# Performance work log

Measured on AMD Instinct MI355X. Metric: run time of the kernel, lower is better.

The kernel has to match this reference:

```python
import jax, jax.numpy as jnp
import numpy as np

D_MODEL = 256
D_INNER = 512   # expand_factor * d_model
D_STATE = 64
DT_RANK = 4     # ceil(d_model / 64)
D_CONV = 4
B = 8
L = 144


def setup_inputs() -> dict:
    key = jax.random.key(0)
    ks = jax.random.split(key, 8)
    s = lambda k, shp, sc=0.02: jax.random.normal(k, shp, jnp.float32) * sc
    x = jax.random.normal(ks[0], (B, L, D_MODEL), jnp.float32)
    lastin = jnp.zeros((B, D_INNER, D_STATE), jnp.float32)  # accepted but unused by the scan
    W_in = s(ks[1], (2 * D_INNER, D_MODEL))              # in_proj (no bias)
    conv_w = s(ks[2], (D_INNER, 1, D_CONV), 0.1)          # depthwise conv kernel [O, I/groups, K]
    conv_b = jnp.zeros((D_INNER,), jnp.float32)
    W_x = s(ks[3], (DT_RANK + 2 * D_STATE, D_INNER))      # x_proj (no bias)
    W_dt = s(ks[4], (D_INNER, DT_RANK), 0.1)
    b_dt = jnp.full((D_INNER,), -4.0, jnp.float32)        # softplus -> small dt, like mamba init
    A_log = jnp.log(jnp.tile(jnp.arange(1, D_STATE + 1, dtype=jnp.float32), (D_INNER, 1)))
    Dp = jnp.ones((D_INNER,), jnp.float32)
    W_out = s(ks[5], (D_MODEL, D_INNER))                  # out_proj (no bias)
    return dict(x=x, lastin=lastin, W_in=W_in, conv_w=conv_w, conv_b=conv_b,
                W_x=W_x, W_dt=W_dt, b_dt=b_dt, A_log=A_log, Dp=Dp, W_out=W_out)


def _forward(x, lastin, W_in, conv_w, conv_b, W_x, W_dt, b_dt, A_log, Dp, W_out):
    # in_proj and split
    xz = jnp.einsum('bld,ed->ble', x, W_in)               # [B, L, 2*d_inner]
    ix, z = jnp.split(xz, 2, axis=-1)

    # depthwise causal-ish conv1d: torch padding=2 then slice [:L] == padding (2, 1)
    ix = jnp.swapaxes(ix, 1, 2)                            # [B, d_inner, L]
    ix = jax.lax.conv_general_dilated(
        ix, conv_w, window_strides=(1,), padding=[(2, 1)],
        feature_group_count=D_INNER, dimension_numbers=('NCH', 'OIH', 'NCH'))
    ix = ix + conv_b[None, :, None]
    ix = jnp.swapaxes(ix, 1, 2)                            # [B, L, d_inner]
    ix = jax.nn.silu(ix)

    # ssm parameterization
    A = -jnp.exp(A_log)                                    # [d_inner, d_state]
    dBC = jnp.einsum('bld,ed->ble', ix, W_x)               # [B, L, dt_rank + 2*d_state]
    dt_r = dBC[..., :DT_RANK]
    Bm = dBC[..., DT_RANK:DT_RANK + D_STATE]               # [B, L, d_state]
    Cm = dBC[..., DT_RANK + D_STATE:]                      # [B, L, d_state]
    delta = jax.nn.softplus(jnp.einsum('blr,dr->bld', dt_r, W_dt) + b_dt)  # [B, L, d_inner]

    # discretization
    deltaA = jnp.exp(delta[..., None] * A)                 # [B, L, d_inner, d_state]
    BX = (delta * ix)[..., None] * Bm[:, :, None, :]       # [B, L, d_inner, d_state]

    # sequential selective scan: h_t = deltaA_t * h_{t-1} + BX_t
    def step(h, inp):
        dA_t, bx_t = inp
        h = dA_t * h + bx_t
        return h, h

    h0 = jnp.zeros((x.shape[0], D_INNER, D_STATE), x.dtype)
    _, hs = jax.lax.scan(step, h0, (jnp.moveaxis(deltaA, 1, 0), jnp.moveaxis(BX, 1, 0)))
    # hs: [L, B, d_inner, d_state]

    y = jnp.einsum('lbdn,lbn->bld', hs, jnp.moveaxis(Cm, 1, 0))  # [B, L, d_inner]
    y = y + Dp * ix

    out = jnp.einsum('bld,ed->ble', y * jax.nn.silu(z), W_out)   # [B, L, d_model]
    return out


def reference(x, lastin, W_in, conv_w, conv_b, W_x, W_dt, b_dt, A_log, Dp, W_out):
    return _forward(x, lastin, W_in, conv_w, conv_b, W_x, W_dt, b_dt, A_log, Dp, W_out)
```

## Files before the change

### kernel.cpp

```cpp
#include <hip/hip_runtime.h>
#include <hip/hip_bf16.h>

#define B_SZ 8
#define L_SEQ 144
#define NTOK 1152
#define D_MODEL 256
#define D_INNER 512
#define D_STATE 64
#define DT_RANK 4

#define BM 64
#define BN 64
#define BK 16

template<bool A_MK, bool B_NK, bool GN>
__global__ __launch_bounds__(256) void gemm_k(const float* __restrict__ A,
                                              const float* __restrict__ Bm,
                                              float* __restrict__ C,
                                              const int M, const int N, const int K,
                                              const int lda, const int ldb, const int ldc,
                                              const int kslab, const size_t sstride) {
    __shared__ float As[BK][BM + 4];
    __shared__ float Bs[BK][BN + 4];
    const int tid = threadIdx.x;
    const int m0 = blockIdx.y * BM;
    const int n0 = blockIdx.x * BN;
    const int kbeg = blockIdx.z * kslab;
    const int kend = kbeg + kslab;
    const int ty = tid >> 4, tx = tid & 15;
    const int lrow = tid >> 2, kq = (tid & 3) * 4;
    const int kk = tid >> 4, cc = (tid & 15) * 4;
    float acc[4][4] = {};

    for (int k0 = kbeg; k0 < kend; k0 += BK) {
        float4 av, bv;
        if (A_MK) av = *(const float4*)(A + (size_t)(m0 + lrow) * lda + k0 + kq);
        else      av = *(const float4*)(A + (size_t)(k0 + kk) * lda + m0 + cc);
        if (B_NK) {
            bv = *(const float4*)(Bm + (size_t)(k0 + kk) * ldb + n0 + cc);
        } else {
            bv = make_float4(0.f, 0.f, 0.f, 0.f);
            if (!GN || (n0 + lrow) < N)
                bv = *(const float4*)(Bm + (size_t)(n0 + lrow) * ldb + k0 + kq);
        }
        __syncthreads();
        if (A_MK) {
            As[kq + 0][lrow] = av.x; As[kq + 1][lrow] = av.y;
            As[kq + 2][lrow] = av.z; As[kq + 3][lrow] = av.w;
        } else {
            *(float4*)&As[kk][cc] = av;
        }
        if (B_NK) {
            *(float4*)&Bs[kk][cc] = bv;
        } else {
            Bs[kq + 0][lrow] = bv.x; Bs[kq + 1][lrow] = bv.y;
            Bs[kq + 2][lrow] = bv.z; Bs[kq + 3][lrow] = bv.w;
        }
        __syncthreads();
#pragma unroll
        for (int k = 0; k < BK; ++k) {
            const float4 a4 = *(const float4*)&As[k][ty * 4];
            const float4 b4 = *(const float4*)&Bs[k][tx * 4];
            const float a_[4] = {a4.x, a4.y, a4.z, a4.w};
            const float b_[4] = {b4.x, b4.y, b4.z, b4.w};
#pragma unroll
            for (int i = 0; i < 4; ++i)
#pragma unroll
                for (int j = 0; j < 4; ++j)
                    acc[i][j] = fmaf(a_[i], b_[j], acc[i][j]);
        }
    }
    C += (size_t)blockIdx.z * sstride;
#pragma unroll
    for (int i = 0; i < 4; ++i) {
        const int gm = m0 + ty * 4 + i;
        const int gn = n0 + tx * 4;
        if (!GN || gn < N)
            *(float4*)(C + (size_t)gm * ldc + gn) =
                make_float4(acc[i][0], acc[i][1], acc[i][2], acc[i][3]);
    }
}

__global__ __launch_bounds__(256) void reduce4_k(const float4* __restrict__ in,
                                                 float4* __restrict__ out,
                                                 const int n4, const int s4) {
    const int i = blockIdx.x * 256 + threadIdx.x;
    if (i >= n4) return;
    const float4 a = in[i], b = in[i + s4], c = in[i + 2 * s4], d = in[i + 3 * s4];
    out[i] = make_float4(a.x + b.x + c.x + d.x, a.y + b.y + c.y + d.y,
                         a.z + b.z + c.z + d.z, a.w + b.w + c.w + d.w);
}

__global__ __launch_bounds__(128) void conv_k(const float* __restrict__ xzT,
                                              const float* __restrict__ cw,
                                              const float* __restrict__ cb,
                                              float* __restrict__ ixT) {
    const int tok = blockIdx.x * 128 + threadIdx.x;
    const int d = blockIdx.y;
    const int b = tok / L_SEQ;
    const int t = tok - b * L_SEQ;
    const float* row = xzT + (size_t)d * NTOK + tok;
    const float4 w = *(const float4*)(cw + d * 4);
    float s = cb[d];
    if (t >= 2) s = fmaf(w.x, row[-2], s);
    if (t >= 1) s = fmaf(w.y, row[-1], s);
    s = fmaf(w.z, row[0], s);
    if (t < L_SEQ - 1) s = fmaf(w.w, row[1], s);
    ixT[(size_t)d * NTOK + tok] = s * __builtin_amdgcn_rcpf(1.f + __expf(-s));
}

template<int CNT>
__device__ __forceinline__ void scan_chunk(const float* __restrict__ dBC,
                                           const float* __restrict__ xzT,
                                           const float* __restrict__ ixT,
                                           float* __restrict__ gT,
                                           float4* __restrict__ aux_w,
                                           float (*__restrict__ Pw)[65],
                                           const int d, const int base, const int t0,
                                           const float An2, const float4 wdt,
                                           const float bdt, const float dpv,
                                           const int lane, float& h) {
    if (lane < CNT) {
        const int tok = base + t0 + lane;
        const float4 dt4 = *(const float4*)(dBC + (size_t)tok * 132);
        float s = fmaf(dt4.x, wdt.x, bdt);
        s = fmaf(dt4.y, wdt.y, s);
        s = fmaf(dt4.z, wdt.z, s);
        s = fmaf(dt4.w, wdt.w, s);
        const float delta = fmaxf(s, 0.f) + __logf(1.f + __expf(-fabsf(s)));
        const float ixv = ixT[(size_t)d * NTOK + tok];
        const float zv  = xzT[(size_t)(D_INNER + d) * NTOK + tok];
        const float sz  = zv * __builtin_amdgcn_rcpf(1.f + __expf(-zv));
        aux_w[lane] = make_float4(delta, delta * ixv, dpv * ixv, sz);
    }
#pragma unroll 8
    for (int i = 0; i < CNT; ++i) {
        const size_t rb = (size_t)(base + t0 + i) * 132;
        const float Bv = dBC[rb + DT_RANK + lane];
        const float Cv = dBC[rb + DT_RANK + D_STATE + lane];
        const float4 a4 = aux_w[i];
        const float dA = __builtin_amdgcn_exp2f(a4.x * An2);
        h = fmaf(dA, h, a4.y * Bv);
        Pw[i][lane] = h * Cv;
    }
    const int tl = lane & 31, hf = lane >> 5;
    float s2 = 0.f;
    if (tl < CNT) {
#pragma unroll
        for (int j = 0; j < 32; ++j) s2 += Pw[tl][hf * 32 + j];
    }
    s2 += __shfl_xor(s2, 32, 64);
    if (hf == 0 && tl < CNT) {
        const float4 a4 = aux_w[tl];
        gT[(size_t)d * NTOK + base + t0 + tl] = (s2 + a4.z) * a4.w;
    }
}

__global__ __launch_bounds__(256) void scan_k(const float* __restrict__ dBC,
                                              const float* __restrict__ xzT,
                                              const float* __restrict__ ixT,
                                              const float* __restrict__ W_dt,
                                              const float* __restrict__ b_dt,
                                              const float* __restrict__ A_log,
                                              const float* __restrict__ Dp,
                                              float* __restrict__ gT) {
    __shared__ float4 aux_s[4][32];
    __shared__ float P[4][32][65];
    const int w = threadIdx.x >> 6, lane = threadIdx.x & 63;
    const int b = blockIdx.x >> 7, dg = blockIdx.x & 127;
    const int d = (dg << 2) | w;
    const int base = b * L_SEQ;
    const float An2 = -__expf(A_log[(d << 6) + lane]) * 1.44269504088896f;
    const float4 wdt = *(const float4*)(W_dt + (d << 2));
    const float bdt = b_dt[d], dpv = Dp[d];
    float h = 0.f;
    scan_chunk<32>(dBC, xzT, ixT, gT, aux_s[w], P[w], d, base, 0,  An2, wdt, bdt, dpv, lane, h);
    scan_chunk<32>(dBC, xzT, ixT, gT, aux_s[w], P[w], d, base, 32, An2, wdt, bdt, dpv, lane, h);
    scan_chunk<32>(dBC, xzT, ixT, gT, aux_s[w], P[w], d, base, 64, An2, wdt, bdt, dpv, lane, h);
    scan_chunk<32>(dBC, xzT, ixT, gT, aux_s[w], P[w], d, base, 96, An2, wdt, bdt, dpv, lane, h);
    scan_chunk<16>(dBC, xzT, ixT, gT, aux_s[w], P[w], d, base, 128, An2, wdt, bdt, dpv, lane, h);
}

extern "C" void kernel_launch(void* const* d_in, const int* in_sizes, int n_in,
                              void* d_out, int out_size, void* d_ws, size_t ws_size,
                              hipStream_t stream) {
    const float* x      = (const float*)d_in[0];
    const float* W_in   = (const float*)d_in[2];
    const float* conv_w = (const float*)d_in[3];
    const float* conv_b = (const float*)d_in[4];
    const float* W_x    = (const float*)d_in[5];
    const float* W_dt   = (const float*)d_in[6];
    const float* b_dt   = (const float*)d_in[7];
    const float* A_log  = (const float*)d_in[8];
    const float* Dp     = (const float*)d_in[9];
    const float* W_out  = (const float*)d_in[10];
    float* out = (float*)d_out;

    float* ws    = (float*)d_ws;
    float* xzT   = ws;
    float* ixT   = xzT + 1179648;
    float* dBC   = ixT + 589824;
    float* gT    = dBC + 152064;
    float* slab3 = gT + 589824;
    float* slab6 = xzT;

    gemm_k<true, false, false><<<dim3(18, 16, 1), 256, 0, stream>>>(
        W_in, x, xzT, 1024, NTOK, D_MODEL, D_MODEL, D_MODEL, NTOK, D_MODEL, 0);
    conv_k<<<dim3(9, D_INNER), 128, 0, stream>>>(xzT, conv_w, conv_b, ixT);
    gemm_k<false, false, true><<<dim3(3, 18, 4), 256, 0, stream>>>(
        ixT, W_x, slab3, NTOK, 132, D_INNER, NTOK, D_INNER, 132, 128, (size_t)NTOK * 132);
    reduce4_k<<<dim3(149), 256, 0, stream>>>((const float4*)slab3, (float4*)dBC,
                                             NTOK * 132 / 4, NTOK * 132 / 4);
    scan_k<<<dim3(B_SZ * 128), 256, 0, stream>>>(dBC, xzT, ixT, W_dt, b_dt, A_log, Dp, gT);
    gemm_k<false, false, false><<<dim3(4, 18, 4), 256, 0, stream>>>(
        gT, W_out, slab6, NTOK, D_MODEL, D_INNER, NTOK, D_INNER, D_MODEL, 128,
        (size_t)NTOK * D_MODEL);
    reduce4_k<<<dim3(288), 256, 0, stream>>>((const float4*)slab6, (float4*)out,
                                             NTOK * D_MODEL / 4, NTOK * D_MODEL / 4);
}
```

Baseline: 142.5 us.

## Fuse all stages into one cooperative persistent kernel with grid syncs

Replaces the seven separate launches with a single cooperative kernel that walks the in_proj GEMM, conv, x_proj GEMM, reduction, scan, out_proj GEMM and final reduction as grid-strided job loops separated by grid.sync. The goal is to remove per-launch overhead and inter-kernel gaps. The change also adds register prefetch of the next K-tile in the GEMM tile and uses 8-way split-K instead of 4-way for the two smaller GEMMs. Grid barriers and persistent-grid occupancy limits may cost more than the launch gaps they remove. A fallback multi-kernel path stays in place for when the cooperative launch fails.

```diff
diff --git a/kernel.cpp b/kernel.cpp
--- a/kernel.cpp
+++ b/kernel.cpp
@@ -1,5 +1,7 @@
 #include <hip/hip_runtime.h>
-#include <hip/hip_bf16.h>
+#include <hip/hip_cooperative_groups.h>
+
+namespace cg = cooperative_groups;
 
 #define B_SZ 8
 #define L_SEQ 144
@@ -8,41 +10,34 @@
 #define D_INNER 512
 #define D_STATE 64
 #define DT_RANK 4
+#define NDBC 132
 
 #define BM 64
 #define BN 64
 #define BK 16
 
-template<bool A_MK, bool B_NK, bool GN>
-__global__ __launch_bounds__(256) void gemm_k(const float* __restrict__ A,
-                                              const float* __restrict__ Bm,
-                                              float* __restrict__ C,
-                                              const int M, const int N, const int K,
-                                              const int lda, const int ldb, const int ldc,
-                                              const int kslab, const size_t sstride) {
-    __shared__ float As[BK][BM + 4];
-    __shared__ float Bs[BK][BN + 4];
-    const int tid = threadIdx.x;
-    const int m0 = blockIdx.y * BM;
-    const int n0 = blockIdx.x * BN;
-    const int kbeg = blockIdx.z * kslab;
-    const int kend = kbeg + kslab;
+template<bool A_MK, bool GN>
+__device__ __forceinline__ void gemm_tile(const float* __restrict__ A,
+                                          const float* __restrict__ Bm,
+                                          float* __restrict__ C,
+                                          const int N, const int lda, const int ldb,
+                                          const int ldc, const int m0, const int n0,
+                                          const int kbeg, const int kend,
+                                          float (*__restrict__ As)[BM + 4],
+                                          float (*__restrict__ Bs)[BN + 4],
+                                          const int tid) {
     const int ty = tid >> 4, tx = tid & 15;
     const int lrow = tid >> 2, kq = (tid & 3) * 4;
     const int kk = tid >> 4, cc = (tid & 15) * 4;
     float acc[4][4] = {};
+    float4 av, bv;
+    if (A_MK) av = *(const float4*)(A + (size_t)(m0 + lrow) * lda + kbeg + kq);
+    else      av = *(const float4*)(A + (size_t)(kbeg + kk) * lda + m0 + cc);
+    bv = make_float4(0.f, 0.f, 0.f, 0.f);
+    if (!GN || (n0 + lrow) < N)
+        bv = *(const float4*)(Bm + (size_t)(n0 + lrow) * ldb + kbeg + kq);
 
     for (int k0 = kbeg; k0 < kend; k0 += BK) {
-        float4 av, bv;
-        if (A_MK) av = *(const float4*)(A + (size_t)(m0 + lrow) * lda + k0 + kq);
-        else      av = *(const float4*)(A + (size_t)(k0 + kk) * lda + m0 + cc);
-        if (B_NK) {
-            bv = *(const float4*)(Bm + (size_t)(k0 + kk) * ldb + n0 + cc);
-        } else {
-            bv = make_float4(0.f, 0.f, 0.f, 0.f);
-            if (!GN || (n0 + lrow) < N)
-                bv = *(const float4*)(Bm + (size_t)(n0 + lrow) * ldb + k0 + kq);
-        }
         __syncthreads();
         if (A_MK) {
             As[kq + 0][lrow] = av.x; As[kq + 1][lrow] = av.y;
@@ -50,13 +45,16 @@
         } else {
             *(float4*)&As[kk][cc] = av;
         }
-        if (B_NK) {
-            *(float4*)&Bs[kk][cc] = bv;
-        } else {
-            Bs[kq + 0][lrow] = bv.x; Bs[kq + 1][lrow] = bv.y;
-            Bs[kq + 2][lrow] = bv.z; Bs[kq + 3][lrow] = bv.w;
-        }
+        Bs[kq + 0][lrow] = bv.x; Bs[kq + 1][lrow] = bv.y;
+        Bs[kq + 2][lrow] = bv.z; Bs[kq + 3][lrow] = bv.w;
         __syncthreads();
+        const int k1 = k0 + BK;
+        if (k1 < kend) {
+            if (A_MK) av = *(const float4*)(A + (size_t)(m0 + lrow) * lda + k1 + kq);
+            else      av = *(const float4*)(A + (size_t)(k1 + kk) * lda + m0 + cc);
+            if (!GN || (n0 + lrow) < N)
+                bv = *(const float4*)(Bm + (size_t)(n0 + lrow) * ldb + k1 + kq);
+        }
 #pragma unroll
         for (int k = 0; k < BK; ++k) {
             const float4 a4 = *(const float4*)&As[k][ty * 4];
@@ -70,7 +68,6 @@
                     acc[i][j] = fmaf(a_[i], b_[j], acc[i][j]);
         }
     }
-    C += (size_t)blockIdx.z * sstride;
 #pragma unroll
     for (int i = 0; i < 4; ++i) {
         const int gm = m0 + ty * 4 + i;
@@ -79,6 +76,180 @@
             *(float4*)(C + (size_t)gm * ldc + gn) =
                 make_float4(acc[i][0], acc[i][1], acc[i][2], acc[i][3]);
     }
+}
+
+template<int CNT>
+__device__ __forceinline__ void scan_chunk(const float* __restrict__ dBC,
+                                           const float* __restrict__ xzT,
+                                           const float* __restrict__ ixT,
+                                           float* __restrict__ gT,
+                                           float4* __restrict__ aux_w,
+                                           float (*__restrict__ Pw)[65],
+                                           const int d, const int base, const int t0,
+                                           const float An2, const float4 wdt,
+                                           const float bdt, const float dpv,
+                                           const int lane, float& h) {
+    if (lane < CNT) {
+        const int tok = base + t0 + lane;
+        const float4 dt4 = *(const float4*)(dBC + (size_t)tok * NDBC);
+        float s = fmaf(dt4.x, wdt.x, bdt);
+        s = fmaf(dt4.y, wdt.y, s);
+        s = fmaf(dt4.z, wdt.z, s);
+        s = fmaf(dt4.w, wdt.w, s);
+        const float delta = fmaxf(s, 0.f) + __logf(1.f + __expf(-fabsf(s)));
+        const float ixv = ixT[(size_t)d * NTOK + tok];
+        const float zv  = xzT[(size_t)(D_INNER + d) * NTOK + tok];
+        const float sz  = zv * __builtin_amdgcn_rcpf(1.f + __expf(-zv));
+        aux_w[lane] = make_float4(delta, delta * ixv, dpv * ixv, sz);
+    }
+#pragma unroll 8
+    for (int i = 0; i < CNT; ++i) {
+        const size_t rb = (size_t)(base + t0 + i) * NDBC;
+        const float Bv = dBC[rb + DT_RANK + lane];
+        const float Cv = dBC[rb + DT_RANK + D_STATE + lane];
+        const float4 a4 = aux_w[i];
+        const float dA = __builtin_amdgcn_exp2f(a4.x * An2);
+        h = fmaf(dA, h, a4.y * Bv);
+        Pw[i][lane] = h * Cv;
+    }
+    const int tl = lane & 31, hf = lane >> 5;
+    float s2 = 0.f;
+    if (tl < CNT) {
+#pragma unroll
+        for (int j = 0; j < 32; ++j) s2 += Pw[tl][hf * 32 + j];
+    }
+    s2 += __shfl_xor(s2, 32, 64);
+    if (hf == 0 && tl < CNT) {
+        const float4 a4 = aux_w[tl];
+        gT[(size_t)d * NTOK + base + t0 + tl] = (s2 + a4.z) * a4.w;
+    }
+}
+
+union MegaSmem {
+    struct { float As[BK][BM + 4]; float Bs[BK][BN + 4]; } g;
+    struct { float4 aux[4][32]; float P[4][32][65]; } s;
+};
+
+__global__ __launch_bounds__(256, 4) void mega_k(
+    const float* __restrict__ x,      const float* __restrict__ W_in,
+    const float* __restrict__ conv_w, const float* __restrict__ conv_b,
+    const float* __restrict__ W_x,    const float* __restrict__ W_dt,
+    const float* __restrict__ b_dt,   const float* __restrict__ A_log,
+    const float* __restrict__ Dp,     const float* __restrict__ W_out,
+    float* __restrict__ out,          float* __restrict__ ws) {
+    __shared__ MegaSmem sm;
+    cg::grid_group grid = cg::this_grid();
+    const int tid = threadIdx.x;
+    const int bid = blockIdx.x;
+    const int nb  = gridDim.x;
+
+    float* xzT = ws;
+    float* ixT = xzT + 1179648;
+    float* dBC = ixT + 589824;
+    float* gT  = dBC + 152064;
+    float* sl3 = gT + 589824;
+    float* sl6 = sl3 + 8 * 152064;
+
+    for (int job = bid; job < 288; job += nb)
+        gemm_tile<true, false>(W_in, x, xzT, NTOK, D_MODEL, D_MODEL, NTOK,
+                               (job / 18) * BM, (job % 18) * BN, 0, D_MODEL,
+                               sm.g.As, sm.g.Bs, tid);
+    grid.sync();
+
+    for (int idx = bid * 256 + tid; idx < D_INNER * NTOK; idx += nb * 256) {
+        const int dd = idx / NTOK, tok = idx - dd * NTOK;
+        const int bb = tok / L_SEQ, t = tok - bb * L_SEQ;
+        const float* row = xzT + (size_t)dd * NTOK + tok;
+        const float4 wv = *(const float4*)(conv_w + dd * 4);
+        float s = conv_b[dd];
+        if (t >= 2) s = fmaf(wv.x, row[-2], s);
+        if (t >= 1) s = fmaf(wv.y, row[-1], s);
+        s = fmaf(wv.z, row[0], s);
+        if (t < L_SEQ - 1) s = fmaf(wv.w, row[1], s);
+        ixT[idx] = s * __builtin_amdgcn_rcpf(1.f + __expf(-s));
+    }
+    grid.sync();
+
+    for (int job = bid; job < 432; job += nb) {
+        const int sK = job / 54, r = job % 54;
+        gemm_tile<false, true>(ixT, W_x, sl3 + (size_t)sK * 152064, NDBC,
+                               NTOK, D_INNER, NDBC,
+                               (r / 3) * BM, (r % 3) * BN, sK * 64, sK * 64 + 64,
+                               sm.g.As, sm.g.Bs, tid);
+    }
+    grid.sync();
+
+    {
+        const float4* in4 = (const float4*)sl3;
+        float4* o4 = (float4*)dBC;
+        for (int i = bid * 256 + tid; i < 38016; i += nb * 256) {
+            float4 a = in4[i];
+#pragma unroll
+            for (int sK = 1; sK < 8; ++sK) {
+                const float4 bb = in4[i + sK * 38016];
+                a.x += bb.x; a.y += bb.y; a.z += bb.z; a.w += bb.w;
+            }
+            o4[i] = a;
+        }
+    }
+    grid.sync();
+
+    {
+        const int w = tid >> 6, lane = tid & 63;
+        for (int unit = bid; unit < B_SZ * 128; unit += nb) {
+            const int bb = unit >> 7, dg = unit & 127;
+            const int d = (dg << 2) | w;
+            const int base = bb * L_SEQ;
+            const float An2 = -__expf(A_log[(d << 6) + lane]) * 1.44269504088896f;
+            const float4 wdt = *(const float4*)(W_dt + (d << 2));
+            const float bdt = b_dt[d], dpv = Dp[d];
+            float h = 0.f;
+            scan_chunk<32>(dBC, xzT, ixT, gT, sm.s.aux[w], sm.s.P[w], d, base, 0,   An2, wdt, bdt, dpv, lane, h);
+            scan_chunk<32>(dBC, xzT, ixT, gT, sm.s.aux[w], sm.s.P[w], d, base, 32,  An2, wdt, bdt, dpv, lane, h);
+            scan_chunk<32>(dBC, xzT, ixT, gT, sm.s.aux[w], sm.s.P[w], d, base, 64,  An2, wdt, bdt, dpv, lane, h);
+            scan_chunk<32>(dBC, xzT, ixT, gT, sm.s.aux[w], sm.s.P[w], d, base, 96,  An2, wdt, bdt, dpv, lane, h);
+            scan_chunk<16>(dBC, xzT, ixT, gT, sm.s.aux[w], sm.s.P[w], d, base, 128, An2, wdt, bdt, dpv, lane, h);
+        }
+    }
+    grid.sync();
+
+    for (int job = bid; job < 576; job += nb) {
+        const int sK = job / 72, r = job % 72;
+        gemm_tile<false, false>(gT, W_out, sl6 + (size_t)sK * 294912, D_MODEL,
+                                NTOK, D_INNER, D_MODEL,
+                                (r / 4) * BM, (r % 4) * BN, sK * 64, sK * 64 + 64,
+                                sm.g.As, sm.g.Bs, tid);
+    }
+    grid.sync();
+
+    {
+        const float4* in4 = (const float4*)sl6;
+        float4* o4 = (float4*)out;
+        for (int i = bid * 256 + tid; i < 73728; i += nb * 256) {
+            float4 a = in4[i];
+#pragma unroll
+            for (int sK = 1; sK < 8; ++sK) {
+                const float4 bb = in4[i + sK * 73728];
+                a.x += bb.x; a.y += bb.y; a.z += bb.z; a.w += bb.w;
+            }
+            o4[i] = a;
+        }
+    }
+}
+
+template<bool A_MK, bool GN>
+__global__ __launch_bounds__(256) void gemm_k2(const float* __restrict__ A,
+                                               const float* __restrict__ Bm,
+                                               float* __restrict__ C,
+                                               const int N, const int lda, const int ldb,
+                                               const int ldc, const int kslab,
+                                               const size_t sstride) {
+    __shared__ float As[BK][BM + 4];
+    __shared__ float Bs[BK][BN + 4];
+    gemm_tile<A_MK, GN>(A, Bm, C + (size_t)blockIdx.z * sstride, N, lda, ldb, ldc,
+                        blockIdx.y * BM, blockIdx.x * BN,
+                        blockIdx.z * kslab, blockIdx.z * kslab + kslab,
+                        As, Bs, (int)threadIdx.x);
 }
 
 __global__ __launch_bounds__(256) void reduce4_k(const float4* __restrict__ in,
@@ -107,53 +278,6 @@
     s = fmaf(w.z, row[0], s);
     if (t < L_SEQ - 1) s = fmaf(w.w, row[1], s);
     ixT[(size_t)d * NTOK + tok] = s * __builtin_amdgcn_rcpf(1.f + __expf(-s));
-}
-
-template<int CNT>
-__device__ __forceinline__ void scan_chunk(const float* __restrict__ dBC,
-                                           const float* __restrict__ xzT,
-                                           const float* __restrict__ ixT,
-                                           float* __restrict__ gT,
-                                           float4* __restrict__ aux_w,
-                                           float (*__restrict__ Pw)[65],
-                                           const int d, const int base, const int t0,
-                                           const float An2, const float4 wdt,
-                                           const float bdt, const float dpv,
-                                           const int lane, float& h) {
-    if (lane < CNT) {
-        const int tok = base + t0 + lane;
-        const float4 dt4 = *(const float4*)(dBC + (size_t)tok * 132);
-        float s = fmaf(dt4.x, wdt.x, bdt);
-        s = fmaf(dt4.y, wdt.y, s);
-        s = fmaf(dt4.z, wdt.z, s);
-        s = fmaf(dt4.w, wdt.w, s);
-        const float delta = fmaxf(s, 0.f) + __logf(1.f + __expf(-fabsf(s)));
-        const float ixv = ixT[(size_t)d * NTOK + tok];
-        const float zv  = xzT[(size_t)(D_INNER + d) * NTOK + tok];
-        const float sz  = zv * __builtin_amdgcn_rcpf(1.f + __expf(-zv));
-        aux_w[lane] = make_float4(delta, delta * ixv, dpv * ixv, sz);
-    }
-#pragma unroll 8
-    for (int i = 0; i < CNT; ++i) {
-        const size_t rb = (size_t)(base + t0 + i) * 132;
-        const float Bv = dBC[rb + DT_RANK + lane];
-        const float Cv = dBC[rb + DT_RANK + D_STATE + lane];
-        const float4 a4 = aux_w[i];
-        const float dA = __builtin_amdgcn_exp2f(a4.x * An2);
-        h = fmaf(dA, h, a4.y * Bv);
-        Pw[i][lane] = h * Cv;
-    }
-    const int tl = lane & 31, hf = lane >> 5;
-    float s2 = 0.f;
-    if (tl < CNT) {
-#pragma unroll
-        for (int j = 0; j < 32; ++j) s2 += Pw[tl][hf * 32 + j];
-    }
-    s2 += __shfl_xor(s2, 32, 64);
-    if (hf == 0 && tl < CNT) {
-        const float4 a4 = aux_w[tl];
-        gT[(size_t)d * NTOK + base + t0 + tl] = (s2 + a4.z) * a4.w;
-    }
 }
 
 __global__ __launch_bounds__(256) void scan_k(const float* __restrict__ dBC,
@@ -174,10 +298,10 @@
     const float4 wdt = *(const float4*)(W_dt + (d << 2));
     const float bdt = b_dt[d], dpv = Dp[d];
     float h = 0.f;
-    scan_chunk<32>(dBC, xzT, ixT, gT, aux_s[w], P[w], d, base, 0,  An2, wdt, bdt, dpv, lane, h);
-    scan_chunk<32>(dBC, xzT, ixT, gT, aux_s[w], P[w], d, base, 32, An2, wdt, bdt, dpv, lane, h);
-    scan_chunk<32>(dBC, xzT, ixT, gT, aux_s[w], P[w], d, base, 64, An2, wdt, bdt, dpv, lane, h);
-    scan_chunk<32>(dBC, xzT, ixT, gT, aux_s[w], P[w], d, base, 96, An2, wdt, bdt, dpv, lane, h);
+    scan_chunk<32>(dBC, xzT, ixT, gT, aux_s[w], P[w], d, base, 0,   An2, wdt, bdt, dpv, lane, h);
+    scan_chunk<32>(dBC, xzT, ixT, gT, aux_s[w], P[w], d, base, 32,  An2, wdt, bdt, dpv, lane, h);
+    scan_chunk<32>(dBC, xzT, ixT, gT, aux_s[w], P[w], d, base, 64,  An2, wdt, bdt, dpv, lane, h);
+    scan_chunk<32>(dBC, xzT, ixT, gT, aux_s[w], P[w], d, base, 96,  An2, wdt, bdt, dpv, lane, h);
     scan_chunk<16>(dBC, xzT, ixT, gT, aux_s[w], P[w], d, base, 128, An2, wdt, bdt, dpv, lane, h);
 }
 
@@ -195,26 +319,49 @@
     const float* Dp     = (const float*)d_in[9];
     const float* W_out  = (const float*)d_in[10];
     float* out = (float*)d_out;
-
-    float* ws    = (float*)d_ws;
-    float* xzT   = ws;
-    float* ixT   = xzT + 1179648;
-    float* dBC   = ixT + 589824;
-    float* gT    = dBC + 152064;
-    float* slab3 = gT + 589824;
-    float* slab6 = xzT;
-
-    gemm_k<true, false, false><<<dim3(18, 16, 1), 256, 0, stream>>>(
-        W_in, x, xzT, 1024, NTOK, D_MODEL, D_MODEL, D_MODEL, NTOK, D_MODEL, 0);
+    float* ws  = (float*)d_ws;
+
+    static int grid = -1;
+    if (grid < 0) {
+        int occ = 0;
+        if (hipOccupancyMaxActiveBlocksPerMultiprocessor(&occ, (const void*)mega_k,
+                                                         256, 0) != hipSuccess || occ < 1)
+            occ = 1;
+        int dev = 0;
+        hipGetDevice(&dev);
+        int nCU = 0;
+        if (hipDeviceGetAttribute(&nCU, hipDeviceAttributeMultiprocessorCount, dev)
+                != hipSuccess || nCU < 1)
+            nCU = 256;
+        long g = (long)occ * (long)nCU;
+        grid = (int)(g > 1024 ? 1024 : g);
+        if (grid < 1) grid = 256;
+    }
+
+    void* args[] = { (void*)&x, (void*)&W_in, (void*)&conv_w, (void*)&conv_b,
+                     (void*)&W_x, (void*)&W_dt, (void*)&b_dt, (void*)&A_log,
+                     (void*)&Dp, (void*)&W_out, (void*)&out, (void*)&ws };
+    if (hipLaunchCooperativeKernel((const void*)mega_k, dim3(grid), dim3(256),
+                                   args, 0, stream) == hipSuccess)
+        return;
+
+    float* xzT = ws;
+    float* ixT = xzT + 1179648;
+    float* dBC = ixT + 589824;
+    float* gT  = dBC + 152064;
+    float* sl3 = gT + 589824;
+    float* sl6 = sl3 + 8 * 152064;
+
+    gemm_k2<true, false><<<dim3(18, 16, 1), 256, 0, stream>>>(
+        W_in, x, xzT, NTOK, D_MODEL, D_MODEL, NTOK, D_MODEL, 0);
     conv_k<<<dim3(9, D_INNER), 128, 0, stream>>>(xzT, conv_w, conv_b, ixT);
-    gemm_k<false, false, true><<<dim3(3, 18, 4), 256, 0, stream>>>(
-        ixT, W_x, slab3, NTOK, 132, D_INNER, NTOK, D_INNER, 132, 128, (size_t)NTOK * 132);
-    reduce4_k<<<dim3(149), 256, 0, stream>>>((const float4*)slab3, (float4*)dBC,
-                                             NTOK * 132 / 4, NTOK * 132 / 4);
+    gemm_k2<false, true><<<dim3(3, 18, 4), 256, 0, stream>>>(
+        ixT, W_x, sl3, NDBC, NTOK, D_INNER, NDBC, 128, (size_t)NTOK * NDBC);
+    reduce4_k<<<dim3(149), 256, 0, stream>>>((const float4*)sl3, (float4*)dBC,
+                                             38016, 38016);
     scan_k<<<dim3(B_SZ * 128), 256, 0, stream>>>(dBC, xzT, ixT, W_dt, b_dt, A_log, Dp, gT);
-    gemm_k<false, false, false><<<dim3(4, 18, 4), 256, 0, stream>>>(
-        gT, W_out, slab6, NTOK, D_MODEL, D_INNER, NTOK, D_INNER, D_MODEL, 128,
-        (size_t)NTOK * D_MODEL);
-    reduce4_k<<<dim3(288), 256, 0, stream>>>((const float4*)slab6, (float4*)out,
-                                             NTOK * D_MODEL / 4, NTOK * D_MODEL / 4);
-}
+    gemm_k2<false, false><<<dim3(4, 18, 4), 256, 0, stream>>>(
+        gT, W_out, sl6, D_MODEL, NTOK, D_INNER, D_MODEL, 128, (size_t)NTOK * D_MODEL);
+    reduce4_k<<<dim3(288), 256, 0, stream>>>((const float4*)sl6, (float4*)out,
+                                             73728, 73728);
+}
```

Measured after the change: 501.0 us. 3.51x slower.

## Fuse depthwise conv+SiLU into x_proj GEMM load and scan; prefetch GEMM tiles

Applied to the files above, without the earlier changes.

Removes the standalone conv kernel and the ixT intermediate buffer. The x_proj GEMM now applies the depthwise conv and SiLU while loading its A tile, using neighbour reads within each batch sequence. The scan kernel recomputes the same conv+SiLU per token from xzT. The GEMM also prefetches the next K-tile into registers before computing on the current one, overlapping global loads with FMAs. This saves one launch and a full write/read of the activation, at the cost of redundant exp work across N-blocks and in the scan, plus higher register pressure.

```diff
diff --git a/kernel.cpp b/kernel.cpp
--- a/kernel.cpp
+++ b/kernel.cpp
@@ -1,5 +1,4 @@
 #include <hip/hip_runtime.h>
-#include <hip/hip_bf16.h>
 
 #define B_SZ 8
 #define L_SEQ 144
@@ -8,17 +7,20 @@
 #define D_INNER 512
 #define D_STATE 64
 #define DT_RANK 4
+#define NDBC 132
 
 #define BM 64
 #define BN 64
 #define BK 16
 
-template<bool A_MK, bool B_NK, bool GN>
+template<bool A_MK, bool GN, bool CONV>
 __global__ __launch_bounds__(256) void gemm_k(const float* __restrict__ A,
                                               const float* __restrict__ Bm,
                                               float* __restrict__ C,
-                                              const int M, const int N, const int K,
-                                              const int lda, const int ldb, const int ldc,
+                                              const int N, const int lda, const int ldb,
+                                              const int ldc,
+                                              const float* __restrict__ cw,
+                                              const float* __restrict__ cb,
                                               const int kslab, const size_t sstride) {
     __shared__ float As[BK][BM + 4];
     __shared__ float Bs[BK][BN + 4];
@@ -31,32 +33,60 @@
     const int lrow = tid >> 2, kq = (tid & 3) * 4;
     const int kk = tid >> 4, cc = (tid & 15) * 4;
     float acc[4][4] = {};
-
-    for (int k0 = kbeg; k0 < kend; k0 += BK) {
-        float4 av, bv;
-        if (A_MK) av = *(const float4*)(A + (size_t)(m0 + lrow) * lda + k0 + kq);
-        else      av = *(const float4*)(A + (size_t)(k0 + kk) * lda + m0 + cc);
-        if (B_NK) {
-            bv = *(const float4*)(Bm + (size_t)(k0 + kk) * ldb + n0 + cc);
+    float4 av, bv, cw4;
+    float xm2 = 0.f, xm1 = 0.f, xp4 = 0.f, cbv = 0.f;
+
+    auto loadA = [&](const int k0) {
+        if (A_MK) {
+            av = *(const float4*)(A + (size_t)(m0 + lrow) * lda + k0 + kq);
         } else {
-            bv = make_float4(0.f, 0.f, 0.f, 0.f);
-            if (!GN || (n0 + lrow) < N)
-                bv = *(const float4*)(Bm + (size_t)(n0 + lrow) * ldb + k0 + kq);
+            const float* row = A + (size_t)(k0 + kk) * lda + m0 + cc;
+            av = *(const float4*)row;
+            if (CONV) {
+                const int t = (m0 + cc) % L_SEQ;
+                xm2 = (t > 0) ? row[-2] : 0.f;
+                xm1 = (t > 0) ? row[-1] : 0.f;
+                xp4 = (t < L_SEQ - 4) ? row[4] : 0.f;
+                cw4 = *(const float4*)(cw + (k0 + kk) * 4);
+                cbv = cb[k0 + kk];
+            }
         }
-        __syncthreads();
+        if (!GN || (n0 + lrow) < N)
+            bv = *(const float4*)(Bm + (size_t)(n0 + lrow) * ldb + k0 + kq);
+    };
+
+    auto storeLDS = [&]() {
         if (A_MK) {
             As[kq + 0][lrow] = av.x; As[kq + 1][lrow] = av.y;
             As[kq + 2][lrow] = av.z; As[kq + 3][lrow] = av.w;
+        } else if (CONV) {
+            const float in7[7] = {xm2, xm1, av.x, av.y, av.z, av.w, xp4};
+            float4 o;
+            float* op = &o.x;
+#pragma unroll
+            for (int j = 0; j < 4; ++j) {
+                float s = cbv;
+                s = fmaf(cw4.x, in7[j + 0], s);
+                s = fmaf(cw4.y, in7[j + 1], s);
+                s = fmaf(cw4.z, in7[j + 2], s);
+                s = fmaf(cw4.w, in7[j + 3], s);
+                op[j] = s * __builtin_amdgcn_rcpf(1.f + __expf(-s));
+            }
+            *(float4*)&As[kk][cc] = o;
         } else {
             *(float4*)&As[kk][cc] = av;
         }
-        if (B_NK) {
-            *(float4*)&Bs[kk][cc] = bv;
-        } else {
-            Bs[kq + 0][lrow] = bv.x; Bs[kq + 1][lrow] = bv.y;
-            Bs[kq + 2][lrow] = bv.z; Bs[kq + 3][lrow] = bv.w;
-        }
+        Bs[kq + 0][lrow] = bv.x; Bs[kq + 1][lrow] = bv.y;
+        Bs[kq + 2][lrow] = bv.z; Bs[kq + 3][lrow] = bv.w;
+    };
+
+    bv = make_float4(0.f, 0.f, 0.f, 0.f);
+    loadA(kbeg);
+    for (int k0 = kbeg; k0 < kend; k0 += BK) {
         __syncthreads();
+        storeLDS();
+        __syncthreads();
+        if (k0 + BK < kend) loadA(k0 + BK);
 #pragma unroll
         for (int k = 0; k < BK; ++k) {
             const float4 a4 = *(const float4*)&As[k][ty * 4];
@@ -91,51 +121,41 @@
                          a.z + b.z + c.z + d.z, a.w + b.w + c.w + d.w);
 }
 
-__global__ __launch_bounds__(128) void conv_k(const float* __restrict__ xzT,
-                                              const float* __restrict__ cw,
-                                              const float* __restrict__ cb,
-                                              float* __restrict__ ixT) {
-    const int tok = blockIdx.x * 128 + threadIdx.x;
-    const int d = blockIdx.y;
-    const int b = tok / L_SEQ;
-    const int t = tok - b * L_SEQ;
-    const float* row = xzT + (size_t)d * NTOK + tok;
-    const float4 w = *(const float4*)(cw + d * 4);
-    float s = cb[d];
-    if (t >= 2) s = fmaf(w.x, row[-2], s);
-    if (t >= 1) s = fmaf(w.y, row[-1], s);
-    s = fmaf(w.z, row[0], s);
-    if (t < L_SEQ - 1) s = fmaf(w.w, row[1], s);
-    ixT[(size_t)d * NTOK + tok] = s * __builtin_amdgcn_rcpf(1.f + __expf(-s));
-}
-
 template<int CNT>
 __device__ __forceinline__ void scan_chunk(const float* __restrict__ dBC,
                                            const float* __restrict__ xzT,
-                                           const float* __restrict__ ixT,
                                            float* __restrict__ gT,
                                            float4* __restrict__ aux_w,
                                            float (*__restrict__ Pw)[65],
                                            const int d, const int base, const int t0,
                                            const float An2, const float4 wdt,
                                            const float bdt, const float dpv,
+                                           const float4 cw4, const float cbv,
                                            const int lane, float& h) {
     if (lane < CNT) {
-        const int tok = base + t0 + lane;
-        const float4 dt4 = *(const float4*)(dBC + (size_t)tok * 132);
+        const int t = t0 + lane;
+        const int tok = base + t;
+        const float* row = xzT + (size_t)d * NTOK + tok;
+        float s0 = cbv;
+        if (t >= 2) s0 = fmaf(cw4.x, row[-2], s0);
+        if (t >= 1) s0 = fmaf(cw4.y, row[-1], s0);
+        s0 = fmaf(cw4.z, row[0], s0);
+        if (t < L_SEQ - 1) s0 = fmaf(cw4.w, row[1], s0);
+        const float ixv = s0 * __builtin_amdgcn_rcpf(1.f + __expf(-s0));
+
+        const float4 dt4 = *(const float4*)(dBC + (size_t)tok * NDBC);
         float s = fmaf(dt4.x, wdt.x, bdt);
         s = fmaf(dt4.y, wdt.y, s);
         s = fmaf(dt4.z, wdt.z, s);
         s = fmaf(dt4.w, wdt.w, s);
         const float delta = fmaxf(s, 0.f) + __logf(1.f + __expf(-fabsf(s)));
-        const float ixv = ixT[(size_t)d * NTOK + tok];
-        const float zv  = xzT[(size_t)(D_INNER + d) * NTOK + tok];
-        const float sz  = zv * __builtin_amdgcn_rcpf(1.f + __expf(-zv));
+        const float zv = xzT[(size_t)(D_INNER + d) * NTOK + tok];
+        const float sz = zv * __builtin_amdgcn_rcpf(1.f + __expf(-zv));
         aux_w[lane] = make_float4(delta, delta * ixv, dpv * ixv, sz);
     }
 #pragma unroll 8
     for (int i = 0; i < CNT; ++i) {
-        const size_t rb = (size_t)(base + t0 + i) * 132;
+        const size_t rb = (size_t)(base + t0 + i) * NDBC;
         const float Bv = dBC[rb + DT_RANK + lane];
         const float Cv = dBC[rb + DT_RANK + D_STATE + lane];
         const float4 a4 = aux_w[i];
@@ -158,11 +178,12 @@
 
 __global__ __launch_bounds__(256) void scan_k(const float* __restrict__ dBC,
                                               const float* __restrict__ xzT,
-                                              const float* __restrict__ ixT,
                                               const float* __restrict__ W_dt,
                                               const float* __restrict__ b_dt,
                                               const float* __restrict__ A_log,
                                               const float* __restrict__ Dp,
+                                              const float* __restrict__ conv_w,
+                                              const float* __restrict__ conv_b,
                                               float* __restrict__ gT) {
     __shared__ float4 aux_s[4][32];
     __shared__ float P[4][32][65];
@@ -173,12 +194,14 @@
     const float An2 = -__expf(A_log[(d << 6) + lane]) * 1.44269504088896f;
     const float4 wdt = *(const float4*)(W_dt + (d << 2));
     const float bdt = b_dt[d], dpv = Dp[d];
+    const float4 cw4 = *(const float4*)(conv_w + (d << 2));
+    const float cbv = conv_b[d];
     float h = 0.f;
-    scan_chunk<32>(dBC, xzT, ixT, gT, aux_s[w], P[w], d, base, 0,  An2, wdt, bdt, dpv, lane, h);
-    scan_chunk<32>(dBC, xzT, ixT, gT, aux_s[w], P[w], d, base, 32, An2, wdt, bdt, dpv, lane, h);
-    scan_chunk<32>(dBC, xzT, ixT, gT, aux_s[w], P[w], d, base, 64, An2, wdt, bdt, dpv, lane, h);
-    scan_chunk<32>(dBC, xzT, ixT, gT, aux_s[w], P[w], d, base, 96, An2, wdt, bdt, dpv, lane, h);
-    scan_chunk<16>(dBC, xzT, ixT, gT, aux_s[w], P[w], d, base, 128, An2, wdt, bdt, dpv, lane, h);
+    scan_chunk<32>(dBC, xzT, gT, aux_s[w], P[w], d, base, 0,   An2, wdt, bdt, dpv, cw4, cbv, lane, h);
+    scan_chunk<32>(dBC, xzT, gT, aux_s[w], P[w], d, base, 32,  An2, wdt, bdt, dpv, cw4, cbv, lane, h);
+    scan_chunk<32>(dBC, xzT, gT, aux_s[w], P[w], d, base, 64,  An2, wdt, bdt, dpv, cw4, cbv, lane, h);
+    scan_chunk<32>(dBC, xzT, gT, aux_s[w], P[w], d, base, 96,  An2, wdt, bdt, dpv, cw4, cbv, lane, h);
+    scan_chunk<16>(dBC, xzT, gT, aux_s[w], P[w], d, base, 128, An2, wdt, bdt, dpv, cw4, cbv, lane, h);
 }
 
 extern "C" void kernel_launch(void* const* d_in, const int* in_sizes, int n_in,
@@ -196,25 +219,25 @@
     const float* W_out  = (const float*)d_in[10];
     float* out = (float*)d_out;
 
-    float* ws    = (float*)d_ws;
-    float* xzT   = ws;
-    float* ixT   = xzT + 1179648;
-    float* dBC   = ixT + 589824;
-    float* gT    = dBC + 152064;
-    float* slab3 = gT + 589824;
-    float* slab6 = xzT;
+    float* ws  = (float*)d_ws;
+    float* xzT = ws;
+    float* dBC = xzT + 1179648;
+    float* gT  = dBC + 152064;
+    float* sl3 = gT + 589824;
+    float* sl6 = xzT;
 
     gemm_k<true, false, false><<<dim3(18, 16, 1), 256, 0, stream>>>(
-        W_in, x, xzT, 1024, NTOK, D_MODEL, D_MODEL, D_MODEL, NTOK, D_MODEL, 0);
-    conv_k<<<dim3(9, D_INNER), 128, 0, stream>>>(xzT, conv_w, conv_b, ixT);
-    gemm_k<false, false, true><<<dim3(3, 18, 4), 256, 0, stream>>>(
-        ixT, W_x, slab3, NTOK, 132, D_INNER, NTOK, D_INNER, 132, 128, (size_t)NTOK * 132);
-    reduce4_k<<<dim3(149), 256, 0, stream>>>((const float4*)slab3, (float4*)dBC,
-                                             NTOK * 132 / 4, NTOK * 132 / 4);
-    scan_k<<<dim3(B_SZ * 128), 256, 0, stream>>>(dBC, xzT, ixT, W_dt, b_dt, A_log, Dp, gT);
+        W_in, x, xzT, NTOK, D_MODEL, D_MODEL, NTOK, nullptr, nullptr, D_MODEL, 0);
+    gemm_k<false, true, true><<<dim3(3, 18, 4), 256, 0, stream>>>(
+        xzT, W_x, sl3, NDBC, NTOK, D_INNER, NDBC, conv_w, conv_b, 128,
+        (size_t)NTOK * NDBC);
+    reduce4_k<<<dim3(149), 256, 0, stream>>>((const float4*)sl3, (float4*)dBC,
+                                             NTOK * NDBC / 4, NTOK * NDBC / 4);
+    scan_k<<<dim3(B_SZ * 128), 256, 0, stream>>>(dBC, xzT, W_dt, b_dt, A_log, Dp,
+                                                 conv_w, conv_b, gT);
     gemm_k<false, false, false><<<dim3(4, 18, 4), 256, 0, stream>>>(
-        gT, W_out, slab6, NTOK, D_MODEL, D_INNER, NTOK, D_INNER, D_MODEL, 128,
+        gT, W_out, sl6, D_MODEL, NTOK, D_INNER, D_MODEL, nullptr, nullptr, 128,
         (size_t)NTOK * D_MODEL);
-    reduce4_k<<<dim3(288), 256, 0, stream>>>((const float4*)slab6, (float4*)out,
+    reduce4_k<<<dim3(288), 256, 0, stream>>>((const float4*)sl6, (float4*)out,
                                              NTOK * D_MODEL / 4, NTOK * D_MODEL / 4);
 }
```

After: 138.7 us. -2.7%, faster.
